# Performance work log

Measured on AMD Instinct MI355X. Metric: run time of the kernel, lower is better.

The kernel has to match this reference:

```python
import jax, jax.numpy as jnp
import numpy as np

B, IN_DIM, N_NODES, N_LEAVES, N_ACTIONS = 131072, 128, 511, 512, 16


def setup_inputs() -> dict:
    key = jax.random.key(0)
    k1, k2, k3, k4 = jax.random.split(key, 4)
    x = jax.random.normal(k1, (B, IN_DIM), dtype=jnp.float32)
    W1 = jax.random.normal(k2, (N_NODES, IN_DIM), dtype=jnp.float32) * 0.1
    b1 = jax.random.normal(k3, (N_NODES,), dtype=jnp.float32) * 0.1
    W2 = jax.random.normal(k4, (N_LEAVES, 2 * N_NODES), dtype=jnp.float32) * 0.05
    # leaf -> action assignment; arange % n_actions guarantees every group non-empty
    leaf_actions = (jnp.arange(N_LEAVES) % N_ACTIONS).astype(jnp.int32)
    return {"x": x, "W1": W1, "b1": b1, "W2": W2, "leaf_actions": leaf_actions}


def reference(x, W1, b1, W2, leaf_actions):
    # linear1
    h = x @ W1.T + b1                      # [B, N_NODES]
    # relu(h) || relu(-h)
    z = jnp.concatenate([jax.nn.relu(h), jax.nn.relu(-h)], axis=1)  # [B, 2*N_NODES]
    # linear2 (no bias)
    y = z @ W2.T                           # [B, N_LEAVES]
    # grouped segment-max over leaf columns, grouped by action id
    pooled = jax.ops.segment_max(y.T, leaf_actions, num_segments=N_ACTIONS).T  # [B, N_ACTIONS]
    return jax.nn.softmax(pooled, axis=-1)
```

## Files before the change

kernel.cpp:

```cpp
#include <hip/hip_runtime.h>
#include <hip/hip_bf16.h>

typedef unsigned short u16;
typedef unsigned int u32;
typedef __attribute__((ext_vector_type(8))) short bf16x8;
typedef __attribute__((ext_vector_type(4))) float f32x4;

#define NROWS   131072
#define KDIM    128
#define NNODES  511
#define NPAD    512
#define NACT    16

__device__ __forceinline__ u16 f2b(float v) {
  return __builtin_bit_cast(u16, __float2bfloat16(v));
}

union Frag {
  bf16x8 v;
  u16    u[8];
  int4   i;
  int    d[4];
};

__device__ __forceinline__ u32 encf(float f) {
  u32 b = __builtin_bit_cast(u32, f);
  return (b & 0x80000000u) ? ~b : (b | 0x80000000u);
}
__device__ __forceinline__ float decf(u32 u) {
  u32 b = (u & 0x80000000u) ? (u & 0x7FFFFFFFu) : ~u;
  return __builtin_bit_cast(float, b);
}

__global__ void prep_k(const float* __restrict__ W1, const float* __restrict__ W2,
                       const float* __restrict__ b1, u16* __restrict__ w1f,
                       u16* __restrict__ wdf, u16* __restrict__ wsf,
                       float* __restrict__ b1p, u32* __restrict__ outi) {
  int bid = blockIdx.x, t = threadIdx.x;
  if (bid < 256) {
    int o = bid * 256 + t;
    int j = o & 7, l = (o >> 3) & 63, kb = (o >> 9) & 3, nt = o >> 11;
    int row = nt * 16 + (l & 15);
    int col = kb * 32 + (l >> 4) * 8 + j;
    w1f[o] = f2b((row < NNODES) ? W1[row * KDIM + col] : 0.f);
  } else if (bid < 2304) {
    int isS = (bid >= 1280);
    int o = (bid - (isS ? 1280 : 256)) * 256 + t;
    int j = o & 7, l = (o >> 3) & 63, kb = (o >> 9) & 15, lt = o >> 13;
    int leaf = lt * 16 + (l & 15);
    int n = kb * 32 + (l >> 4) * 8 + j;
    float va = 0.f, vb = 0.f;
    if (n < NNODES) {
      va = W2[leaf * (2 * NNODES) + n];
      vb = W2[leaf * (2 * NNODES) + NNODES + n];
    }
    float v = isS ? 0.5f * (va + vb) : 0.5f * (va - vb);
    (isS ? wsf : wdf)[o] = f2b(v);
  } else if (bid < 2306) {
    int i = (bid - 2304) * 256 + t;
    if (i < NPAD) b1p[i] = (i < NNODES) ? b1[i] : 0.f;
  } else {
    int i = (bid - 2306) * 256 + t;
    ((uint4*)outi)[i] = make_uint4(0u, 0u, 0u, 0u);
  }
}

__global__ __launch_bounds__(256, 2) void gemm1_k(const float* __restrict__ x,
                                                  const u16* __restrict__ w1f,
                                                  const float* __restrict__ b1p,
                                                  u16* __restrict__ hb) {
  __shared__ u16 xs[4 * 4 * 64 * 8];
  __shared__ u16 hs[4 * 16 * 64 * 8];

  int t = threadIdx.x, wq = t >> 6, l = t & 63;
  int rg = blockIdx.x;
  int lm = l & 15, quad = l >> 4;

  {
    const float4* xg = (const float4*)(x + (size_t)rg * 64 * KDIM);
#pragma unroll
    for (int i = 0; i < 8; ++i) {
      int f = i * 256 + t;
      int row = f >> 5, col = (f & 31) * 4;
      float4 v = xg[f];
      ushort4 b;
      b.x = f2b(v.x); b.y = f2b(v.y); b.z = f2b(v.z); b.w = f2b(v.w);
      int rt = row >> 4, kb = col >> 5;
      int lane = (row & 15) + 16 * ((col >> 3) & 3);
      *(ushort4*)&xs[(((rt * 4 + kb) * 64 + lane) * 8) + (col & 7)] = b;
    }
  }
  __syncthreads();

  f32x4 zero4 = {0.f, 0.f, 0.f, 0.f};
  f32x4 acc[4][8];
#pragma unroll
  for (int rt = 0; rt < 4; ++rt)
#pragma unroll
    for (int ct = 0; ct < 8; ++ct) acc[rt][ct] = zero4;

#pragma unroll 1
  for (int kb = 0; kb < 4; ++kb) {
    Frag a[4];
#pragma unroll
    for (int rt = 0; rt < 4; ++rt)
      a[rt].i = *(const int4*)&xs[((rt * 4 + kb) * 64 + l) * 8];
#pragma unroll
    for (int ct = 0; ct < 8; ++ct) {
      Frag b;
      b.i = *(const int4*)(w1f + (((wq * 8 + ct) * 4 + kb) * 64 + l) * 8);
#pragma unroll
      for (int rt = 0; rt < 4; ++rt)
        acc[rt][ct] = __builtin_amdgcn_mfma_f32_16x16x32_bf16(a[rt].v, b.v, acc[rt][ct], 0, 0, 0);
    }
  }

#pragma unroll
  for (int ct = 0; ct < 8; ++ct) {
    int node = (wq * 8 + ct) * 16 + lm;
    float bias = b1p[node];
    int kb2 = node >> 5;
    int lsub = 16 * ((node >> 3) & 3);
    int j2 = node & 7;
#pragma unroll
    for (int rt = 0; rt < 4; ++rt)
#pragma unroll
      for (int r = 0; r < 4; ++r) {
        int rl = quad * 4 + r;
        hs[((rt * 16 + kb2) * 64 + (rl + lsub)) * 8 + j2] = f2b(acc[rt][ct][r] + bias);
      }
  }
  __syncthreads();

  {
    int4* dst = (int4*)(hb + (size_t)rg * 32768);
    const int4* src = (const int4*)hs;
#pragma unroll
    for (int i = 0; i < 16; ++i) dst[i * 256 + t] = src[i * 256 + t];
  }
}

__global__ __launch_bounds__(512, 4) void gemm2_k(const u16* __restrict__ hb,
                                                  const u16* __restrict__ wdf,
                                                  const u16* __restrict__ wsf,
                                                  u32* __restrict__ pooled) {
  __shared__ u16 sb[2][40 * 512];

  int t = threadIdx.x, w = t >> 6, l = t & 63;
  int bid = blockIdx.x;
  int half = (bid >> 3) & 1;
  int rg = (bid & 7) | ((bid >> 4) << 3);
  int rh = w >> 2, wq = w & 3;
  int lm = l & 15, quad = l >> 4;

  const u16* gsrc[5];
#pragma unroll
  for (int i = 0; i < 5; ++i) {
    int f = w * 5 + i;
    const u16* p;
    if (f < 8)       p = hb  + ((size_t)(rg * 8 + f) * 16) * 512;
    else if (f < 24) p = wdf + ((size_t)(half * 16 + (f - 8)) * 16) * 512;
    else             p = wsf + ((size_t)(half * 16 + (f - 24)) * 16) * 512;
    gsrc[i] = p + l * 8;
  }

  f32x4 zero4 = {0.f, 0.f, 0.f, 0.f};
  f32x4 acc[4][4];
#pragma unroll
  for (int rt = 0; rt < 4; ++rt)
#pragma unroll
    for (int ct = 0; ct < 4; ++ct) acc[rt][ct] = zero4;

#pragma unroll
  for (int i = 0; i < 5; ++i) {
    int f = w * 5 + i;
    __builtin_amdgcn_global_load_lds(
        (const __attribute__((address_space(1))) void*)(gsrc[i]),
        (__attribute__((address_space(3))) void*)&sb[0][f * 512], 16, 0, 0);
  }
  __syncthreads();

#pragma unroll 1
  for (int kb = 0; kb < 16; ++kb) {
    int cur = kb & 1;
    if (kb < 15) {
#pragma unroll
      for (int i = 0; i < 5; ++i) {
        int f = w * 5 + i;
        __builtin_amdgcn_global_load_lds(
            (const __attribute__((address_space(1))) void*)(gsrc[i] + (kb + 1) * 512),
            (__attribute__((address_space(3))) void*)&sb[cur ^ 1][f * 512], 16, 0, 0);
      }
    }

    Frag h4[4], wA[4], wB[4];
#pragma unroll
    for (int rt = 0; rt < 4; ++rt)
      h4[rt].i = *(const int4*)&sb[cur][(rh * 4 + rt) * 512 + l * 8];
#pragma unroll
    for (int ct = 0; ct < 4; ++ct)
      wA[ct].i = *(const int4*)&sb[cur][(8 + wq * 4 + ct) * 512 + l * 8];
#pragma unroll
    for (int ct = 0; ct < 4; ++ct)
      wB[ct].i = *(const int4*)&sb[cur][(24 + wq * 4 + ct) * 512 + l * 8];

#pragma unroll
    for (int ct = 0; ct < 4; ++ct)
#pragma unroll
      for (int rt = 0; rt < 4; ++rt)
        acc[rt][ct] = __builtin_amdgcn_mfma_f32_16x16x32_bf16(h4[rt].v, wA[ct].v, acc[rt][ct], 0, 0, 0);
#pragma unroll
    for (int rt = 0; rt < 4; ++rt)
#pragma unroll
      for (int d = 0; d < 4; ++d) h4[rt].d[d] &= 0x7FFF7FFF;
#pragma unroll
    for (int ct = 0; ct < 4; ++ct)
#pragma unroll
      for (int rt = 0; rt < 4; ++rt)
        acc[rt][ct] = __builtin_amdgcn_mfma_f32_16x16x32_bf16(h4[rt].v, wB[ct].v, acc[rt][ct], 0, 0, 0);

    __syncthreads();
  }

#pragma unroll
  for (int rt = 0; rt < 4; ++rt)
#pragma unroll
    for (int r = 0; r < 4; ++r) {
      float mx = acc[rt][0][r];
#pragma unroll
      for (int ct = 1; ct < 4; ++ct) mx = fmaxf(mx, acc[rt][ct][r]);
      int row = rg * 128 + rh * 64 + rt * 16 + quad * 4 + r;
      atomicMax(pooled + row * NACT + lm, encf(mx));
    }
}

__global__ void combine_k(u32* __restrict__ outi) {
  int row = blockIdx.x * 256 + threadIdx.x;
  uint4* p = (uint4*)(outi + (size_t)row * NACT);
  uint4 q[4];
#pragma unroll
  for (int i = 0; i < 4; ++i) q[i] = p[i];
  float v[NACT];
#pragma unroll
  for (int i = 0; i < 4; ++i) {
    v[i * 4 + 0] = decf(q[i].x); v[i * 4 + 1] = decf(q[i].y);
    v[i * 4 + 2] = decf(q[i].z); v[i * 4 + 3] = decf(q[i].w);
  }
  float m = v[0];
#pragma unroll
  for (int a = 1; a < NACT; ++a) m = fmaxf(m, v[a]);
  float s = 0.f;
#pragma unroll
  for (int a = 0; a < NACT; ++a) { float e = __expf(v[a] - m); v[a] = e; s += e; }
  float inv = 1.f / s;
  float4* pf = (float4*)(outi + (size_t)row * NACT);
#pragma unroll
  for (int i = 0; i < 4; ++i) {
    float4 o; o.x = v[i*4+0]*inv; o.y = v[i*4+1]*inv; o.z = v[i*4+2]*inv; o.w = v[i*4+3]*inv;
    pf[i] = o;
  }
}

extern "C" void kernel_launch(void* const* d_in, const int* in_sizes, int n_in,
                              void* d_out, int out_size, void* d_ws, size_t ws_size,
                              hipStream_t stream) {
  const float* x  = (const float*)d_in[0];
  const float* W1 = (const float*)d_in[1];
  const float* b1 = (const float*)d_in[2];
  const float* W2 = (const float*)d_in[3];

  char* ws = (char*)d_ws;
  u16*   hb  = (u16*)ws;
  u16*   w1f = (u16*)(ws + 134217728);
  u16*   wdf = (u16*)(ws + 134217728 + 131072);
  u16*   wsf = (u16*)(ws + 134217728 + 131072 + 524288);
  float* b1p = (float*)(ws + 134217728 + 131072 + 524288 + 524288);

  prep_k   <<<dim3(4354), dim3(256), 0, stream>>>(W1, W2, b1, w1f, wdf, wsf, b1p, (u32*)d_out);
  gemm1_k  <<<dim3(NROWS / 64), dim3(256), 0, stream>>>(x, w1f, b1p, hb);
  gemm2_k  <<<dim3(2048), dim3(512), 0, stream>>>(hb, wdf, wsf, (u32*)d_out);
  combine_k<<<dim3(NROWS / 256), dim3(256), 0, stream>>>((u32*)d_out);
}
```

Measured before the change: 272.0 us.

## Fuse both GEMMs, segment-max and softmax into one kernel with 32x32 MFMA

Replaces the separate gemm1, gemm2, atomic-max and combine kernels with a single fused kernel per 128-row tile. The hidden activations now stay in LDS instead of making a 128 MB bf16 round trip through global memory, and the grouped max and softmax are done in-block, so the atomics and the output zeroing go away. The MFMAs change from 16x16x32 to 32x32x16 with new weight layouts. In exchange, each block streams all of W2 itself, and the large LDS footprint limits occupancy.

```diff
diff --git a/kernel.cpp b/kernel.cpp
--- a/kernel.cpp
+++ b/kernel.cpp
@@ -4,12 +4,11 @@
 typedef unsigned short u16;
 typedef unsigned int u32;
 typedef __attribute__((ext_vector_type(8))) short bf16x8;
-typedef __attribute__((ext_vector_type(4))) float f32x4;
+typedef __attribute__((ext_vector_type(16))) float f32x16;
 
 #define NROWS   131072
 #define KDIM    128
 #define NNODES  511
-#define NPAD    512
 #define NACT    16
 
 __device__ __forceinline__ u16 f2b(float v) {
@@ -23,241 +22,189 @@
   int    d[4];
 };
 
-__device__ __forceinline__ u32 encf(float f) {
-  u32 b = __builtin_bit_cast(u32, f);
-  return (b & 0x80000000u) ? ~b : (b | 0x80000000u);
-}
-__device__ __forceinline__ float decf(u32 u) {
-  u32 b = (u & 0x80000000u) ? (u & 0x7FFFFFFFu) : ~u;
-  return __builtin_bit_cast(float, b);
-}
+#define Z16 {0.f,0.f,0.f,0.f,0.f,0.f,0.f,0.f,0.f,0.f,0.f,0.f,0.f,0.f,0.f,0.f}
 
 __global__ void prep_k(const float* __restrict__ W1, const float* __restrict__ W2,
                        const float* __restrict__ b1, u16* __restrict__ w1f,
-                       u16* __restrict__ wdf, u16* __restrict__ wsf,
-                       float* __restrict__ b1p, u32* __restrict__ outi) {
+                       u16* __restrict__ wgt, float* __restrict__ b1r) {
   int bid = blockIdx.x, t = threadIdx.x;
   if (bid < 256) {
     int o = bid * 256 + t;
-    int j = o & 7, l = (o >> 3) & 63, kb = (o >> 9) & 3, nt = o >> 11;
-    int row = nt * 16 + (l & 15);
-    int col = kb * 32 + (l >> 4) * 8 + j;
-    w1f[o] = f2b((row < NNODES) ? W1[row * KDIM + col] : 0.f);
+    int j = o & 7, l = (o >> 3) & 63, ks = (o >> 9) & 7, nt = o >> 12;
+    int node = nt * 32 + (l & 31);
+    int k = ks * 16 + ((l >> 5) << 3) + j;
+    w1f[o] = f2b(node < NNODES ? W1[node * KDIM + k] : 0.f);
   } else if (bid < 2304) {
-    int isS = (bid >= 1280);
-    int o = (bid - (isS ? 1280 : 256)) * 256 + t;
-    int j = o & 7, l = (o >> 3) & 63, kb = (o >> 9) & 15, lt = o >> 13;
-    int leaf = lt * 16 + (l & 15);
-    int n = kb * 32 + (l >> 4) * 8 + j;
+    int o = (bid - 256) * 256 + t;
+    int j = o & 7, l = (o >> 3) & 63, lt = (o >> 9) & 15, s = o >> 13;
+    int type = s & 1, kstep = s >> 1;
+    int leaf = lt * 32 + (l & 31);
+    int n = kstep * 16 + ((l >> 5) << 3) + j;
     float va = 0.f, vb = 0.f;
     if (n < NNODES) {
       va = W2[leaf * (2 * NNODES) + n];
       vb = W2[leaf * (2 * NNODES) + NNODES + n];
     }
-    float v = isS ? 0.5f * (va + vb) : 0.5f * (va - vb);
-    (isS ? wsf : wdf)[o] = f2b(v);
-  } else if (bid < 2306) {
-    int i = (bid - 2304) * 256 + t;
-    if (i < NPAD) b1p[i] = (i < NNODES) ? b1[i] : 0.f;
+    wgt[o] = f2b(type ? 0.5f * (va + vb) : 0.5f * (va - vb));
   } else {
-    int i = (bid - 2306) * 256 + t;
-    ((uint4*)outi)[i] = make_uint4(0u, 0u, 0u, 0u);
-  }
-}
-
-__global__ __launch_bounds__(256, 2) void gemm1_k(const float* __restrict__ x,
+    int o = (bid - 2304) * 256 + t;
+    int r = o & 15, hi2 = (o >> 4) & 1, nt = o >> 5;
+    int node = nt * 32 + (r & 3) + 8 * (r >> 2) + 4 * hi2;
+    b1r[o] = (node < NNODES) ? b1[node] : 0.f;
+  }
+}
+
+__global__ __launch_bounds__(512, 2) void fused_k(const float* __restrict__ x,
                                                   const u16* __restrict__ w1f,
-                                                  const float* __restrict__ b1p,
-                                                  u16* __restrict__ hb) {
-  __shared__ u16 xs[4 * 4 * 64 * 8];
-  __shared__ u16 hs[4 * 16 * 64 * 8];
-
-  int t = threadIdx.x, wq = t >> 6, l = t & 63;
-  int rg = blockIdx.x;
-  int lm = l & 15, quad = l >> 4;
+                                                  const u16* __restrict__ wgt,
+                                                  const float* __restrict__ b1r,
+                                                  float* __restrict__ out) {
+  __shared__ u16 Hh[4 * 32 * 64 * 8];
+  __shared__ u16 Ss[2 * 16 * 64 * 8];
+
+  const int t = threadIdx.x, w = t >> 6, l = t & 63;
+  const int la = l & 31, hi = l >> 5;
+  const int rg = blockIdx.x;
 
   {
-    const float4* xg = (const float4*)(x + (size_t)rg * 64 * KDIM);
-#pragma unroll
-    for (int i = 0; i < 8; ++i) {
-      int f = i * 256 + t;
-      int row = f >> 5, col = (f & 31) * 4;
-      float4 v = xg[f];
-      ushort4 b;
-      b.x = f2b(v.x); b.y = f2b(v.y); b.z = f2b(v.z); b.w = f2b(v.w);
-      int rt = row >> 4, kb = col >> 5;
-      int lane = (row & 15) + 16 * ((col >> 3) & 3);
-      *(ushort4*)&xs[(((rt * 4 + kb) * 64 + lane) * 8) + (col & 7)] = b;
-    }
-  }
-  __syncthreads();
-
-  f32x4 zero4 = {0.f, 0.f, 0.f, 0.f};
-  f32x4 acc[4][8];
+    const float* xb = x + (size_t)rg * 128 * KDIM;
+#pragma unroll
+    for (int i = 0; i < 4; ++i) {
+      int f = w * 4 + i;
+      int rt = f >> 3, ks = f & 7;
+      const float* src = xb + (rt * 32 + la) * KDIM + ks * 16 + hi * 8;
+      float4 v0 = *(const float4*)src;
+      float4 v1 = *(const float4*)(src + 4);
+      Frag fr;
+      fr.u[0] = f2b(v0.x); fr.u[1] = f2b(v0.y); fr.u[2] = f2b(v0.z); fr.u[3] = f2b(v0.w);
+      fr.u[4] = f2b(v1.x); fr.u[5] = f2b(v1.y); fr.u[6] = f2b(v1.z); fr.u[7] = f2b(v1.w);
+      *(int4*)&Ss[f * 512 + l * 8] = fr.i;
+    }
+  }
+  __syncthreads();
+
+  {
+    const int nt0 = w * 2;
+    Frag a1[16];
+#pragma unroll
+    for (int q = 0; q < 16; ++q)
+      a1[q].i = *(const int4*)(w1f + ((size_t)((nt0 + (q >> 3)) * 8 + (q & 7)) * 64 + l) * 8);
+    float4 bias[2][4];
+#pragma unroll
+    for (int n2 = 0; n2 < 2; ++n2)
+#pragma unroll
+      for (int g = 0; g < 4; ++g)
+        bias[n2][g] = *(const float4*)(b1r + ((nt0 + n2) * 2 + hi) * 16 + g * 4);
+
+#pragma unroll 1
+    for (int rt = 0; rt < 4; ++rt) {
+      f32x16 c0 = Z16, c1 = Z16;
+#pragma unroll
+      for (int ks = 0; ks < 8; ++ks) {
+        Frag b;
+        b.i = *(const int4*)&Ss[(rt * 8 + ks) * 512 + l * 8];
+        c0 = __builtin_amdgcn_mfma_f32_32x32x16_bf16(a1[ks].v, b.v, c0, 0, 0, 0);
+        c1 = __builtin_amdgcn_mfma_f32_32x32x16_bf16(a1[8 + ks].v, b.v, c1, 0, 0, 0);
+      }
+#pragma unroll
+      for (int n2 = 0; n2 < 2; ++n2) {
+        int nt = nt0 + n2;
+#pragma unroll
+        for (int p = 0; p < 8; ++p) {
+          int q = p >> 1, e = p & 1;
+          int r0 = 4 * q + 2 * e;
+          float bv0 = e ? bias[n2][q].z : bias[n2][q].x;
+          float bv1 = e ? bias[n2][q].w : bias[n2][q].y;
+          float v0 = (n2 ? c1[r0]     : c0[r0])     + bv0;
+          float v1 = (n2 ? c1[r0 + 1] : c0[r0 + 1]) + bv1;
+          int n32 = 8 * q + 4 * hi + 2 * e;
+          int c_h = n32 >> 4, jj = n32 & 15;
+          u32 pkv = (u32)f2b(v0) | ((u32)f2b(v1) << 16);
+          *(u32*)&Hh[((rt * 32 + nt * 2 + c_h) * 64 + ((jj >> 3) << 5) + la) * 8 + (jj & 6)] = pkv;
+        }
+      }
+    }
+  }
+  __syncthreads();
+
+#pragma unroll
+  for (int i = 0; i < 2; ++i) {
+    int f = w * 2 + i;
+    __builtin_amdgcn_global_load_lds(
+        (const __attribute__((address_space(1))) void*)(wgt + (size_t)f * 512 + l * 8),
+        (__attribute__((address_space(3))) void*)&Ss[f * 512], 16, 0, 0);
+  }
+  __syncthreads();
+
+  f32x16 acc[4][2] = {{Z16, Z16}, {Z16, Z16}, {Z16, Z16}, {Z16, Z16}};
+  Frag ha[4];
+
+#pragma unroll 1
+  for (int s = 0; s < 64; ++s) {
+    if (s < 63) {
+#pragma unroll
+      for (int i = 0; i < 2; ++i) {
+        int f = w * 2 + i;
+        __builtin_amdgcn_global_load_lds(
+            (const __attribute__((address_space(1))) void*)(wgt + (size_t)((s + 1) * 16 + f) * 512 + l * 8),
+            (__attribute__((address_space(3))) void*)&Ss[((s + 1) & 1) * 8192 + f * 512], 16, 0, 0);
+      }
+    }
+    if (!(s & 1)) {
+      int kstep = s >> 1;
+#pragma unroll
+      for (int rt = 0; rt < 4; ++rt)
+        ha[rt].i = *(const int4*)&Hh[((rt * 32 + kstep) * 64 + l) * 8];
+    } else {
+#pragma unroll
+      for (int rt = 0; rt < 4; ++rt)
+#pragma unroll
+        for (int d = 0; d < 4; ++d) ha[rt].d[d] &= 0x7FFF7FFF;
+    }
+    Frag wb0, wb1;
+    wb0.i = *(const int4*)&Ss[(s & 1) * 8192 + (w * 2 + 0) * 512 + l * 8];
+    wb1.i = *(const int4*)&Ss[(s & 1) * 8192 + (w * 2 + 1) * 512 + l * 8];
+#pragma unroll
+    for (int rt = 0; rt < 4; ++rt) {
+      acc[rt][0] = __builtin_amdgcn_mfma_f32_32x32x16_bf16(ha[rt].v, wb0.v, acc[rt][0], 0, 0, 0);
+      acc[rt][1] = __builtin_amdgcn_mfma_f32_32x32x16_bf16(ha[rt].v, wb1.v, acc[rt][1], 0, 0, 0);
+    }
+    __syncthreads();
+  }
+
+  float* Hred = (float*)Hh;
 #pragma unroll
   for (int rt = 0; rt < 4; ++rt)
 #pragma unroll
-    for (int ct = 0; ct < 8; ++ct) acc[rt][ct] = zero4;
-
-#pragma unroll 1
-  for (int kb = 0; kb < 4; ++kb) {
-    Frag a[4];
-#pragma unroll
-    for (int rt = 0; rt < 4; ++rt)
-      a[rt].i = *(const int4*)&xs[((rt * 4 + kb) * 64 + l) * 8];
-#pragma unroll
-    for (int ct = 0; ct < 8; ++ct) {
-      Frag b;
-      b.i = *(const int4*)(w1f + (((wq * 8 + ct) * 4 + kb) * 64 + l) * 8);
-#pragma unroll
-      for (int rt = 0; rt < 4; ++rt)
-        acc[rt][ct] = __builtin_amdgcn_mfma_f32_16x16x32_bf16(a[rt].v, b.v, acc[rt][ct], 0, 0, 0);
-    }
-  }
-
-#pragma unroll
-  for (int ct = 0; ct < 8; ++ct) {
-    int node = (wq * 8 + ct) * 16 + lm;
-    float bias = b1p[node];
-    int kb2 = node >> 5;
-    int lsub = 16 * ((node >> 3) & 3);
-    int j2 = node & 7;
-#pragma unroll
-    for (int rt = 0; rt < 4; ++rt)
-#pragma unroll
-      for (int r = 0; r < 4; ++r) {
-        int rl = quad * 4 + r;
-        hs[((rt * 16 + kb2) * 64 + (rl + lsub)) * 8 + j2] = f2b(acc[rt][ct][r] + bias);
-      }
-  }
-  __syncthreads();
-
+    for (int r = 0; r < 16; ++r) {
+      int row = rt * 32 + (r & 3) + 8 * (r >> 2) + 4 * hi;
+      float v = fmaxf(acc[rt][0][r], acc[rt][1][r]);
+      Hred[(w * 128 + row) * 32 + (la ^ ((r & 3) << 2))] = v;
+    }
+  __syncthreads();
   {
-    int4* dst = (int4*)(hb + (size_t)rg * 32768);
-    const int4* src = (const int4*)hs;
-#pragma unroll
-    for (int i = 0; i < 16; ++i) dst[i * 256 + t] = src[i * 256 + t];
-  }
-}
-
-__global__ __launch_bounds__(512, 4) void gemm2_k(const u16* __restrict__ hb,
-                                                  const u16* __restrict__ wdf,
-                                                  const u16* __restrict__ wsf,
-                                                  u32* __restrict__ pooled) {
-  __shared__ u16 sb[2][40 * 512];
-
-  int t = threadIdx.x, w = t >> 6, l = t & 63;
-  int bid = blockIdx.x;
-  int half = (bid >> 3) & 1;
-  int rg = (bid & 7) | ((bid >> 4) << 3);
-  int rh = w >> 2, wq = w & 3;
-  int lm = l & 15, quad = l >> 4;
-
-  const u16* gsrc[5];
-#pragma unroll
-  for (int i = 0; i < 5; ++i) {
-    int f = w * 5 + i;
-    const u16* p;
-    if (f < 8)       p = hb  + ((size_t)(rg * 8 + f) * 16) * 512;
-    else if (f < 24) p = wdf + ((size_t)(half * 16 + (f - 8)) * 16) * 512;
-    else             p = wsf + ((size_t)(half * 16 + (f - 24)) * 16) * 512;
-    gsrc[i] = p + l * 8;
-  }
-
-  f32x4 zero4 = {0.f, 0.f, 0.f, 0.f};
-  f32x4 acc[4][4];
-#pragma unroll
-  for (int rt = 0; rt < 4; ++rt)
-#pragma unroll
-    for (int ct = 0; ct < 4; ++ct) acc[rt][ct] = zero4;
-
-#pragma unroll
-  for (int i = 0; i < 5; ++i) {
-    int f = w * 5 + i;
-    __builtin_amdgcn_global_load_lds(
-        (const __attribute__((address_space(1))) void*)(gsrc[i]),
-        (__attribute__((address_space(3))) void*)&sb[0][f * 512], 16, 0, 0);
-  }
-  __syncthreads();
-
-#pragma unroll 1
-  for (int kb = 0; kb < 16; ++kb) {
-    int cur = kb & 1;
-    if (kb < 15) {
-#pragma unroll
-      for (int i = 0; i < 5; ++i) {
-        int f = w * 5 + i;
-        __builtin_amdgcn_global_load_lds(
-            (const __attribute__((address_space(1))) void*)(gsrc[i] + (kb + 1) * 512),
-            (__attribute__((address_space(3))) void*)&sb[cur ^ 1][f * 512], 16, 0, 0);
-      }
-    }
-
-    Frag h4[4], wA[4], wB[4];
-#pragma unroll
-    for (int rt = 0; rt < 4; ++rt)
-      h4[rt].i = *(const int4*)&sb[cur][(rh * 4 + rt) * 512 + l * 8];
-#pragma unroll
-    for (int ct = 0; ct < 4; ++ct)
-      wA[ct].i = *(const int4*)&sb[cur][(8 + wq * 4 + ct) * 512 + l * 8];
-#pragma unroll
-    for (int ct = 0; ct < 4; ++ct)
-      wB[ct].i = *(const int4*)&sb[cur][(24 + wq * 4 + ct) * 512 + l * 8];
-
-#pragma unroll
-    for (int ct = 0; ct < 4; ++ct)
-#pragma unroll
-      for (int rt = 0; rt < 4; ++rt)
-        acc[rt][ct] = __builtin_amdgcn_mfma_f32_16x16x32_bf16(h4[rt].v, wA[ct].v, acc[rt][ct], 0, 0, 0);
-#pragma unroll
-    for (int rt = 0; rt < 4; ++rt)
-#pragma unroll
-      for (int d = 0; d < 4; ++d) h4[rt].d[d] &= 0x7FFF7FFF;
-#pragma unroll
-    for (int ct = 0; ct < 4; ++ct)
-#pragma unroll
-      for (int rt = 0; rt < 4; ++rt)
-        acc[rt][ct] = __builtin_amdgcn_mfma_f32_16x16x32_bf16(h4[rt].v, wB[ct].v, acc[rt][ct], 0, 0, 0);
-
-    __syncthreads();
-  }
-
-#pragma unroll
-  for (int rt = 0; rt < 4; ++rt)
-#pragma unroll
-    for (int r = 0; r < 4; ++r) {
-      float mx = acc[rt][0][r];
-#pragma unroll
-      for (int ct = 1; ct < 4; ++ct) mx = fmaxf(mx, acc[rt][ct][r]);
-      int row = rg * 128 + rh * 64 + rt * 16 + quad * 4 + r;
-      atomicMax(pooled + row * NACT + lm, encf(mx));
-    }
-}
-
-__global__ void combine_k(u32* __restrict__ outi) {
-  int row = blockIdx.x * 256 + threadIdx.x;
-  uint4* p = (uint4*)(outi + (size_t)row * NACT);
-  uint4 q[4];
-#pragma unroll
-  for (int i = 0; i < 4; ++i) q[i] = p[i];
-  float v[NACT];
-#pragma unroll
-  for (int i = 0; i < 4; ++i) {
-    v[i * 4 + 0] = decf(q[i].x); v[i * 4 + 1] = decf(q[i].y);
-    v[i * 4 + 2] = decf(q[i].z); v[i * 4 + 3] = decf(q[i].w);
-  }
-  float m = v[0];
-#pragma unroll
-  for (int a = 1; a < NACT; ++a) m = fmaxf(m, v[a]);
-  float s = 0.f;
-#pragma unroll
-  for (int a = 0; a < NACT; ++a) { float e = __expf(v[a] - m); v[a] = e; s += e; }
-  float inv = 1.f / s;
-  float4* pf = (float4*)(outi + (size_t)row * NACT);
-#pragma unroll
-  for (int i = 0; i < 4; ++i) {
-    float4 o; o.x = v[i*4+0]*inv; o.y = v[i*4+1]*inv; o.z = v[i*4+2]*inv; o.w = v[i*4+3]*inv;
-    pf[i] = o;
+    int row = t >> 2, ag = t & 3;
+    int xr = (row & 3) << 2;
+    float p0 = -1e30f, p1 = -1e30f, p2 = -1e30f, p3 = -1e30f;
+#pragma unroll
+    for (int ww = 0; ww < 8; ++ww)
+#pragma unroll
+      for (int h2 = 0; h2 < 2; ++h2) {
+        float4 v = *(const float4*)&Hred[(ww * 128 + row) * 32 + ((h2 * 16 + ag * 4) ^ xr)];
+        p0 = fmaxf(p0, v.x); p1 = fmaxf(p1, v.y);
+        p2 = fmaxf(p2, v.z); p3 = fmaxf(p3, v.w);
+      }
+    float m = fmaxf(fmaxf(p0, p1), fmaxf(p2, p3));
+    m = fmaxf(m, __shfl_xor(m, 1));
+    m = fmaxf(m, __shfl_xor(m, 2));
+    float e0 = __expf(p0 - m), e1 = __expf(p1 - m), e2 = __expf(p2 - m), e3 = __expf(p3 - m);
+    float ssum = e0 + e1 + e2 + e3;
+    ssum += __shfl_xor(ssum, 1);
+    ssum += __shfl_xor(ssum, 2);
+    float inv = 1.f / ssum;
+    float4 o4;
+    o4.x = e0 * inv; o4.y = e1 * inv; o4.z = e2 * inv; o4.w = e3 * inv;
+    *(float4*)(out + ((size_t)rg * 128 + row) * NACT + ag * 4) = o4;
   }
 }
 
@@ -270,14 +217,10 @@
   const float* W2 = (const float*)d_in[3];
 
   char* ws = (char*)d_ws;
-  u16*   hb  = (u16*)ws;
-  u16*   w1f = (u16*)(ws + 134217728);
-  u16*   wdf = (u16*)(ws + 134217728 + 131072);
-  u16*   wsf = (u16*)(ws + 134217728 + 131072 + 524288);
-  float* b1p = (float*)(ws + 134217728 + 131072 + 524288 + 524288);
-
-  prep_k   <<<dim3(4354), dim3(256), 0, stream>>>(W1, W2, b1, w1f, wdf, wsf, b1p, (u32*)d_out);
-  gemm1_k  <<<dim3(NROWS / 64), dim3(256), 0, stream>>>(x, w1f, b1p, hb);
-  gemm2_k  <<<dim3(2048), dim3(512), 0, stream>>>(hb, wdf, wsf, (u32*)d_out);
-  combine_k<<<dim3(NROWS / 256), dim3(256), 0, stream>>>((u32*)d_out);
-}
+  u16*   w1f = (u16*)ws;
+  u16*   wgt = (u16*)(ws + 131072);
+  float* b1r = (float*)(ws + 131072 + 1048576);
+
+  prep_k <<<dim3(2308), dim3(256), 0, stream>>>(W1, W2, b1, w1f, wgt, b1r);
+  fused_k<<<dim3(NROWS / 128), dim3(512), 0, stream>>>(x, w1f, wgt, b1r, (float*)d_out);
+}
```

Result: no change. 267.9 us (-1.5%).
